# Performance work log

Measured on AMD Instinct MI355X. Metric: run time of the kernel, lower is better.

Reference implementation:

```python
import jax, jax.numpy as jnp
import numpy as np

I_DIM, L_DIM, H_DIM, O_DIM = 1024, 1024, 2048, 512
HALT_H = max(4, H_DIM // 2)
BATCH = 4096


def setup_inputs() -> dict:
    key = jax.random.key(0)
    ks = jax.random.split(key, 14)
    s = 0.02
    gin = I_DIM + O_DIM
    jdim = L_DIM + O_DIM
    return {
        "inputs": jax.random.normal(ks[0], (BATCH, I_DIM), jnp.float32),
        "W_ih": jax.random.normal(ks[1], (3 * L_DIM, gin), jnp.float32) * s,
        "W_hh": jax.random.normal(ks[2], (3 * L_DIM, L_DIM), jnp.float32) * s,
        "b_ih": jax.random.normal(ks[3], (3 * L_DIM,), jnp.float32) * s,
        "b_hh": jax.random.normal(ks[4], (3 * L_DIM,), jnp.float32) * s,
        "aw1": jax.random.normal(ks[5], (H_DIM, jdim), jnp.float32) * s,
        "ab1": jax.random.normal(ks[6], (H_DIM,), jnp.float32) * s,
        "aw2": jax.random.normal(ks[7], (O_DIM, H_DIM), jnp.float32) * s,
        "ab2": jax.random.normal(ks[8], (O_DIM,), jnp.float32) * s,
        "hw1": jax.random.normal(ks[9], (HALT_H, jdim), jnp.float32) * s,
        "hb1": jax.random.normal(ks[10], (HALT_H,), jnp.float32) * s,
        "hw2": jax.random.normal(ks[11], (2, HALT_H), jnp.float32) * s,
        "hb2": jax.random.normal(ks[12], (2,), jnp.float32) * s,
        "inner_cycles": 4,
        "outer_steps": 8,
    }


def reference(inputs, W_ih, W_hh, b_ih, b_hh, aw1, ab1, aw2, ab2,
              hw1, hb1, hw2, hb2, inner_cycles, outer_steps):
    B = inputs.shape[0]
    L = W_hh.shape[1]
    O = aw2.shape[0]

    def gru_step(state, x_gates):
        # PyTorch GRUCell: gates ordered (r, z, n)
        h_gates = state @ W_hh.T + b_hh  # [B, 3L]
        xr, xz, xn = jnp.split(x_gates, 3, axis=-1)
        hr, hz, hn = jnp.split(h_gates, 3, axis=-1)
        r = jax.nn.sigmoid(xr + hr)
        z = jax.nn.sigmoid(xz + hz)
        n = jnp.tanh(xn + r * hn)
        return (1.0 - z) * n + z * state

    def outer(carry, _):
        state, ans = carry
        # gru_input is constant over inner cycles -> hoist input projection
        x = jnp.concatenate([inputs, ans], axis=-1)       # [B, I+O]
        x_gates = x @ W_ih.T + b_ih                        # [B, 3L]

        def inner(s, _):
            return gru_step(s, x_gates), None

        state, _ = jax.lax.scan(inner, state, None, length=inner_cycles)
        joint = jnp.concatenate([state, ans], axis=-1)     # [B, L+O]
        h1 = jax.nn.relu(joint @ aw1.T + ab1)
        logits = h1 @ aw2.T + ab2                          # [B, O]
        ans_new = jnp.tanh(logits)
        h2 = jax.nn.relu(joint @ hw1.T + hb1)
        halt = h2 @ hw2.T + hb2                            # [B, 2]
        return (state, ans_new), (logits, halt)

    state0 = jnp.zeros((B, L), inputs.dtype)
    ans0 = jnp.zeros((B, O), inputs.dtype)
    _, (answer_logits, halt_logits) = jax.lax.scan(
        outer, (state0, ans0), None, length=outer_steps)
    # stacked equivalents of the per-step lists: [outer_steps, B, O], [outer_steps, B, 2]
    return answer_logits, halt_logits
```

## Files before the change

kernel.cpp:

```cpp
#include <hip/hip_runtime.h>
#include <math.h>

#define BATCH 4096
#define LDIM 1024
#define HDIM 2048
#define ODIM 512
#define GDIM 3072
#define JDIM 1536
#define INNER 4
#define OUTER 8

using f16 = _Float16;
using f16x4 = __attribute__((ext_vector_type(4))) _Float16;
using f16x8 = __attribute__((ext_vector_type(8))) _Float16;
using f32x4 = __attribute__((ext_vector_type(4))) float;

typedef __attribute__((address_space(3))) void lds_void;
typedef __attribute__((address_space(1))) void glob_void;

__device__ __forceinline__ void gload16(const void* g, void* l) {
  __builtin_amdgcn_global_load_lds((const glob_void*)g, (lds_void*)l, 16, 0, 0);
}

#define MFMA16(a, b, c) __builtin_amdgcn_mfma_f32_16x16x32_f16(a, b, c, 0, 0, 0)
#define WAIT_VM(N) asm volatile("s_waitcnt vmcnt(" #N ")" ::: "memory")

__device__ __forceinline__ float fast_sigmoid(float x) {
  return __builtin_amdgcn_rcpf(1.0f + __expf(-x));
}
__device__ __forceinline__ float fast_tanh(float x) {
  return 1.0f - 2.0f * __builtin_amdgcn_rcpf(1.0f + __expf(2.0f * x));
}

__global__ __launch_bounds__(256) void convert_w(const float* __restrict__ src,
                                                 f16* __restrict__ dst, int n4) {
  int i = blockIdx.x * 256 + threadIdx.x;
  if (i >= n4) return;
  float4 v = ((const float4*)src)[i];
  f16x4 d = {(f16)v.x, (f16)v.y, (f16)v.z, (f16)v.w};
  *(f16x4*)&dst[(size_t)i * 4] = d;
}

__global__ __launch_bounds__(256) void input_to_cat(
    const float* __restrict__ inp, f16* __restrict__ cH) {
  int idx = blockIdx.x * 256 + threadIdx.x;
  if (idx >= BATCH * 256) return;
  int row = idx >> 8, c4 = idx & 255;
  float4 v = ((const float4*)inp)[idx];
  f16x4 h4 = {(f16)v.x, (f16)v.y, (f16)v.z, (f16)v.w};
  *(f16x4*)&cH[(size_t)row * JDIM + c4 * 4] = h4;
}

template <int EPI>
__global__ __launch_bounds__(256, 2) void gemm_f16(
    const f16* __restrict__ A, const f16* __restrict__ W,
    const float* __restrict__ bias, const float* __restrict__ bias2,
    f16* __restrict__ Ch, float* __restrict__ Cf, float* __restrict__ Cout,
    f16* __restrict__ aXH, f16* __restrict__ aJH, int N, int K) {
  __shared__ f16 sA[3][128 * 32];
  __shared__ f16 sW[3][128 * 32];
  const int tid = threadIdx.x;
  const int w = tid >> 6, lane = tid & 63;
  const int wm = w >> 1, wn = w & 1;
  const int fr = lane & 15, quad = lane >> 4;
  const int m0 = blockIdx.y * 128, n0 = blockIdx.x * 128;
  const int srow = w * 32 + (lane >> 2);
  const int scol = (((lane & 3) ^ ((lane >> 3) & 3)) * 8);
  const f16* pA = A + (size_t)(m0 + srow) * K + scol;
  const f16* pW = W + (size_t)(n0 + srow) * K + scol;
  const size_t rstep = (size_t)16 * K;
  const int lo = w * 1024;

  f32x4 acc[4][4] = {};
  const int NT = K >> 5;

  auto stage = [&](int b, int k) {
    gload16(pA + k, &sA[b][lo]);
    gload16(pA + rstep + k, &sA[b][lo + 512]);
    gload16(pW + k, &sW[b][lo]);
    gload16(pW + rstep + k, &sW[b][lo + 512]);
  };
  stage(0, 0);
  stage(1, 32);
  int bb = 0;
  for (int t = 0; t < NT; ++t) {
    if (t == NT - 1) { WAIT_VM(0); } else { WAIT_VM(4); }
    __builtin_amdgcn_s_barrier();
    if (t + 2 < NT) {
      int bn = bb + 2; if (bn >= 3) bn -= 3;
      stage(bn, (t + 2) * 32);
    }
    f16x8 af[4], bf[4];
#pragma unroll
    for (int i = 0; i < 4; ++i) {
      int rr = wm * 64 + i * 16 + fr;
      af[i] = *(const f16x8*)&sA[bb][rr * 32 + ((quad ^ ((rr >> 1) & 3)) << 3)];
    }
#pragma unroll
    for (int j = 0; j < 4; ++j) {
      int rr = wn * 64 + j * 16 + fr;
      bf[j] = *(const f16x8*)&sW[bb][rr * 32 + ((quad ^ ((rr >> 1) & 3)) << 3)];
    }
    __builtin_amdgcn_s_setprio(1);
#pragma unroll
    for (int i = 0; i < 4; ++i)
#pragma unroll
      for (int j = 0; j < 4; ++j) acc[i][j] = MFMA16(af[i], bf[j], acc[i][j]);
    __builtin_amdgcn_s_setprio(0);
    if (++bb == 3) bb = 0;
  }

  bool is_h1 = true;
  const float* bp = bias;
  int nb0 = n0;
  if (EPI == 1) {
    is_h1 = (n0 < 2048);
    bp = is_h1 ? bias : bias2;
    nb0 = is_h1 ? n0 : n0 - 2048;
  }
#pragma unroll
  for (int j = 0; j < 4; ++j) {
    int n = nb0 + wn * 64 + j * 16 + fr;
    float bv = bp[n];
#pragma unroll
    for (int i = 0; i < 4; ++i) {
      int mb = m0 + wm * 64 + i * 16 + quad * 4;
      if (EPI == 0) {
        f16x4 o = {(f16)(acc[i][j][0] + bv), (f16)(acc[i][j][1] + bv),
                   (f16)(acc[i][j][2] + bv), (f16)(acc[i][j][3] + bv)};
        *(f16x4*)&Ch[((size_t)(mb >> 2) * N + n) * 4] = o;
      } else {
#pragma unroll
        for (int r = 0; r < 4; ++r) {
          int m = mb + r;
          float v = acc[i][j][r] + bv;
          if (EPI == 1) {
            float vr = fmaxf(v, 0.0f);
            if (is_h1)
              Ch[(size_t)m * HDIM + n] = (f16)vr;
            else
              Cf[(size_t)m * LDIM + n] = vr;
          } else {
            Cout[(size_t)m * N + n] = v;
            f16 t = (f16)fast_tanh(v);
            size_t c = (size_t)m * JDIM + 1024 + n;
            aXH[c] = t;
            aJH[c] = t;
          }
        }
      }
    }
  }
}

__global__ __launch_bounds__(256, 2) void gru_fused(
    const f16* __restrict__ inH, const f16* __restrict__ Whh,
    const float* __restrict__ bhh, const f16* __restrict__ xgP,
    f16* __restrict__ outH, f16* __restrict__ catJH) {
  __shared__ f16 sA[3][128 * 32];
  __shared__ f16 sW0[3][64 * 32];
  __shared__ f16 sW1[3][64 * 32];
  __shared__ f16 sW2[3][64 * 32];
  const int tid = threadIdx.x;
  const int w = tid >> 6, lane = tid & 63;
  const int fr = lane & 15, quad = lane >> 4;
  const int n0 = blockIdx.x * 64, m0 = blockIdx.y * 128;
  const int srow = w * 32 + (lane >> 2);
  const int scol = (((lane & 3) ^ ((lane >> 3) & 3)) * 8);
  const f16* pA = inH + (size_t)(m0 + srow) * LDIM + scol;
  const size_t rstepA = (size_t)16 * LDIM;
  const int wrow = w * 16 + (lane >> 2);
  const f16* pW0 = Whh + (size_t)(n0 + wrow) * LDIM + scol;
  const f16* pW1 = pW0 + (size_t)LDIM * LDIM;
  const f16* pW2 = pW1 + (size_t)LDIM * LDIM;
  const int loA = w * 1024, loW = w * 512;

  f32x4 ar[2][4] = {}, az[2][4] = {}, an_[2][4] = {};
  const int NT = LDIM >> 5;

  auto stage = [&](int b, int k) {
    gload16(pA + k, &sA[b][loA]);
    gload16(pA + rstepA + k, &sA[b][loA + 512]);
    gload16(pW0 + k, &sW0[b][loW]);
    gload16(pW1 + k, &sW1[b][loW]);
    gload16(pW2 + k, &sW2[b][loW]);
  };
  stage(0, 0);
  stage(1, 32);
  int bb = 0;
  for (int t = 0; t < NT; ++t) {
    if (t == NT - 1) { WAIT_VM(0); } else { WAIT_VM(5); }
    __builtin_amdgcn_s_barrier();
    if (t + 2 < NT) {
      int bn = bb + 2; if (bn >= 3) bn -= 3;
      stage(bn, (t + 2) * 32);
    }
    f16x8 a_[2], w0[4], w1[4], w2[4];
#pragma unroll
    for (int i = 0; i < 2; ++i) {
      int rr = w * 32 + i * 16 + fr;
      a_[i] = *(const f16x8*)&sA[bb][rr * 32 + ((quad ^ ((rr >> 1) & 3)) << 3)];
    }
#pragma unroll
    for (int j = 0; j < 4; ++j) {
      int rw = j * 16 + fr;
      int wo = rw * 32 + ((quad ^ ((rw >> 1) & 3)) << 3);
      w0[j] = *(const f16x8*)&sW0[bb][wo];
      w1[j] = *(const f16x8*)&sW1[bb][wo];
      w2[j] = *(const f16x8*)&sW2[bb][wo];
    }
    __builtin_amdgcn_s_setprio(1);
#pragma unroll
    for (int i = 0; i < 2; ++i)
#pragma unroll
      for (int j = 0; j < 4; ++j) {
        ar[i][j] = MFMA16(a_[i], w0[j], ar[i][j]);
        az[i][j] = MFMA16(a_[i], w1[j], az[i][j]);
        an_[i][j] = MFMA16(a_[i], w2[j], an_[i][j]);
      }
    __builtin_amdgcn_s_setprio(0);
    if (++bb == 3) bb = 0;
  }

#pragma unroll
  for (int j = 0; j < 4; ++j) {
    int col = n0 + j * 16 + fr;
    float br = bhh[col], bz = bhh[col + LDIM], bn = bhh[col + 2 * LDIM];
#pragma unroll
    for (int i = 0; i < 2; ++i) {
      int mb = m0 + w * 32 + i * 16 + quad * 4;
      size_t xb = ((size_t)(mb >> 2) * GDIM + col) * 4;
      f16x4 x4r = *(const f16x4*)&xgP[xb];
      f16x4 x4z = *(const f16x4*)&xgP[xb + (size_t)LDIM * 4];
      f16x4 x4n = *(const f16x4*)&xgP[xb + (size_t)2 * LDIM * 4];
#pragma unroll
      for (int r = 0; r < 4; ++r) {
        int m = mb + r;
        size_t si = (size_t)m * LDIM + col;
        float sold = (float)inH[si];
        float rg = fast_sigmoid((float)x4r[r] + ar[i][j][r] + br);
        float zg = fast_sigmoid((float)x4z[r] + az[i][j][r] + bz);
        float ng = fast_tanh((float)x4n[r] + rg * (an_[i][j][r] + bn));
        float o = (1.0f - zg) * ng + zg * sold;
        f16 oh = (f16)o;
        outH[si] = oh;
        if (catJH) catJH[(size_t)m * JDIM + col] = oh;
      }
    }
  }
}

__global__ __launch_bounds__(256) void halt_kernel(
    const float* __restrict__ h2, const float* __restrict__ hw2,
    const float* __restrict__ hb2, float* __restrict__ out) {
  int wave = (blockIdx.x * 256 + threadIdx.x) >> 6;
  int lane = threadIdx.x & 63;
  if (wave >= BATCH) return;
  const float* row = h2 + (size_t)wave * LDIM;
  float s0 = 0.0f, s1 = 0.0f;
#pragma unroll
  for (int k = lane; k < LDIM; k += 64) {
    float v = row[k];
    s0 = fmaf(v, hw2[k], s0);
    s1 = fmaf(v, hw2[LDIM + k], s1);
  }
#pragma unroll
  for (int off = 32; off > 0; off >>= 1) {
    s0 += __shfl_xor(s0, off);
    s1 += __shfl_xor(s1, off);
  }
  if (lane == 0) {
    out[(size_t)wave * 2 + 0] = s0 + hb2[0];
    out[(size_t)wave * 2 + 1] = s1 + hb2[1];
  }
}

extern "C" void kernel_launch(void* const* d_in, const int* in_sizes, int n_in,
                              void* d_out, int out_size, void* d_ws, size_t ws_size,
                              hipStream_t stream) {
  const float* inputs = (const float*)d_in[0];
  const float* W_ih = (const float*)d_in[1];
  const float* W_hh = (const float*)d_in[2];
  const float* b_ih = (const float*)d_in[3];
  const float* b_hh = (const float*)d_in[4];
  const float* aw1 = (const float*)d_in[5];
  const float* ab1 = (const float*)d_in[6];
  const float* aw2 = (const float*)d_in[7];
  const float* ab2 = (const float*)d_in[8];
  const float* hw1 = (const float*)d_in[9];
  const float* hb1 = (const float*)d_in[10];
  const float* hw2 = (const float*)d_in[11];
  const float* hb2 = (const float*)d_in[12];

  float* out = (float*)d_out;
  float* logits_out = out;
  float* halt_out = out + (size_t)OUTER * BATCH * ODIM;

  char* p = (char*)d_ws;
  auto take = [&](size_t bytes) { char* q = p; p += (bytes + 255) & ~255ull; return q; };
  f16* stA = (f16*)take((size_t)BATCH * LDIM * 2);
  f16* stB = (f16*)take((size_t)BATCH * LDIM * 2);
  f16* catX = (f16*)take((size_t)BATCH * JDIM * 2);
  f16* catJ = (f16*)take((size_t)BATCH * JDIM * 2);
  f16* xg = (f16*)take((size_t)BATCH * GDIM * 2);
  float* h2F = (float*)take((size_t)BATCH * LDIM * 4);
  f16* WihF = (f16*)take((size_t)GDIM * JDIM * 2);
  f16* WhhF = (f16*)take((size_t)GDIM * LDIM * 2);
  f16* WjF = (f16*)take((size_t)(HDIM + LDIM) * JDIM * 2);
  f16* aw2F = (f16*)take((size_t)ODIM * HDIM * 2);
  f16* h1 = xg;

  (void)hipMemsetAsync(stA, 0, (size_t)BATCH * LDIM * 2, stream);
  (void)hipMemsetAsync(catX, 0, (size_t)BATCH * JDIM * 2, stream);
  (void)hipMemsetAsync(catJ, 0, (size_t)BATCH * JDIM * 2, stream);

  auto conv = [&](const float* s, f16* d, size_t n) {
    int n4 = (int)(n / 4);
    convert_w<<<(n4 + 255) / 256, 256, 0, stream>>>(s, d, n4);
  };
  conv(W_ih, WihF, (size_t)GDIM * JDIM);
  conv(W_hh, WhhF, (size_t)GDIM * LDIM);
  conv(aw1, WjF, (size_t)HDIM * JDIM);
  conv(hw1, WjF + (size_t)HDIM * JDIM, (size_t)LDIM * JDIM);
  conv(aw2, aw2F, (size_t)ODIM * HDIM);
  input_to_cat<<<BATCH, 256, 0, stream>>>(inputs, catX);

  for (int s = 0; s < OUTER; ++s) {
    gemm_f16<0><<<dim3(GDIM / 128, BATCH / 128), 256, 0, stream>>>(
        catX, WihF, b_ih, nullptr, xg, nullptr, nullptr, nullptr, nullptr,
        GDIM, JDIM);
    f16 *cur = stA, *nxt = stB;
    for (int c = 0; c < INNER; ++c) {
      bool last = (c == INNER - 1);
      gru_fused<<<dim3(LDIM / 64, BATCH / 128), 256, 0, stream>>>(
          cur, WhhF, b_hh, xg, nxt, last ? catJ : nullptr);
      f16* t = cur; cur = nxt; nxt = t;
    }
    gemm_f16<1><<<dim3((HDIM + LDIM) / 128, BATCH / 128), 256, 0, stream>>>(
        catJ, WjF, ab1, hb1, h1, h2F, nullptr, nullptr, nullptr,
        HDIM + LDIM, JDIM);
    gemm_f16<2><<<dim3(ODIM / 128, BATCH / 128), 256, 0, stream>>>(
        h1, aw2F, ab2, nullptr, nullptr, nullptr,
        logits_out + (size_t)s * BATCH * ODIM, catX, catJ, ODIM, HDIM);
    halt_kernel<<<BATCH / 4, 256, 0, stream>>>(
        h2F, hw2, hb2, halt_out + (size_t)s * BATCH * 2);
  }
}
```

Baseline: 2.726 ms.

## Enlarge GEMM tiles to 256x128 and remap blocks for XCD-local weight reuse

The main f16 GEMM now uses 256x128 block tiles with 8x4 MFMA accumulators per wave, doubling A-tile reuse per weight load. Block indices are flattened and remapped so each XCD handles a contiguous set of N columns, improving L2 locality of weight tiles; the GRU kernel gets the same XCD-aware remap. The logits GEMM is split into its own kernel keeping the 128x128 tile. Larger tiles raise register and LDS usage, which may reduce occupancy, and 384 blocks may leave the grid less evenly balanced across CUs.

```diff
diff --git a/kernel.cpp b/kernel.cpp
--- a/kernel.cpp
+++ b/kernel.cpp
@@ -55,7 +55,103 @@
 __global__ __launch_bounds__(256, 2) void gemm_f16(
     const f16* __restrict__ A, const f16* __restrict__ W,
     const float* __restrict__ bias, const float* __restrict__ bias2,
-    f16* __restrict__ Ch, float* __restrict__ Cf, float* __restrict__ Cout,
+    f16* __restrict__ Ch, float* __restrict__ Cf, int N, int K) {
+  __shared__ f16 sA[3][256 * 32];
+  __shared__ f16 sW[3][128 * 32];
+  const int tid = threadIdx.x;
+  const int w = tid >> 6, lane = tid & 63;
+  const int wm = w >> 1, wn = w & 1;
+  const int fr = lane & 15, quad = lane >> 4;
+  const int flat = blockIdx.x;
+  const int xcd = flat & 7, local = flat >> 3;
+  const int n0 = (xcd * 3 + local % 3) * 128;
+  const int m0 = (local / 3) * 256;
+  const int srowA = w * 64 + (lane >> 2);
+  const int srowW = w * 32 + (lane >> 2);
+  const int scol = (((lane & 3) ^ ((lane >> 3) & 3)) * 8);
+  const f16* pA = A + (size_t)(m0 + srowA) * K + scol;
+  const f16* pW = W + (size_t)(n0 + srowW) * K + scol;
+  const size_t rstep = (size_t)16 * K;
+  const int loA = w * 2048, loW = w * 1024;
+
+  f32x4 acc[8][4] = {};
+  const int NT = K >> 5;
+
+  auto stage = [&](int b, int k) {
+    gload16(pA + k, &sA[b][loA]);
+    gload16(pA + rstep + k, &sA[b][loA + 512]);
+    gload16(pA + 2 * rstep + k, &sA[b][loA + 1024]);
+    gload16(pA + 3 * rstep + k, &sA[b][loA + 1536]);
+    gload16(pW + k, &sW[b][loW]);
+    gload16(pW + rstep + k, &sW[b][loW + 512]);
+  };
+  stage(0, 0);
+  stage(1, 32);
+  int bb = 0;
+  for (int t = 0; t < NT; ++t) {
+    if (t == NT - 1) { WAIT_VM(0); } else { WAIT_VM(6); }
+    __builtin_amdgcn_s_barrier();
+    if (t + 2 < NT) {
+      int bn = bb + 2; if (bn >= 3) bn -= 3;
+      stage(bn, (t + 2) * 32);
+    }
+    f16x8 af[8], bf[4];
+#pragma unroll
+    for (int i = 0; i < 8; ++i) {
+      int rr = wm * 128 + i * 16 + fr;
+      af[i] = *(const f16x8*)&sA[bb][rr * 32 + ((quad ^ ((rr >> 1) & 3)) << 3)];
+    }
+#pragma unroll
+    for (int j = 0; j < 4; ++j) {
+      int rr = wn * 64 + j * 16 + fr;
+      bf[j] = *(const f16x8*)&sW[bb][rr * 32 + ((quad ^ ((rr >> 1) & 3)) << 3)];
+    }
+    __builtin_amdgcn_s_setprio(1);
+#pragma unroll
+    for (int i = 0; i < 8; ++i)
+#pragma unroll
+      for (int j = 0; j < 4; ++j) acc[i][j] = MFMA16(af[i], bf[j], acc[i][j]);
+    __builtin_amdgcn_s_setprio(0);
+    if (++bb == 3) bb = 0;
+  }
+
+  bool is_h1 = true;
+  const float* bp = bias;
+  int nb0 = n0;
+  if (EPI == 1) {
+    is_h1 = (n0 < 2048);
+    bp = is_h1 ? bias : bias2;
+    nb0 = is_h1 ? n0 : n0 - 2048;
+  }
+#pragma unroll
+  for (int j = 0; j < 4; ++j) {
+    int n = nb0 + wn * 64 + j * 16 + fr;
+    float bv = bp[n];
+#pragma unroll
+    for (int i = 0; i < 8; ++i) {
+      int mb = m0 + wm * 128 + i * 16 + quad * 4;
+      if (EPI == 0) {
+        f16x4 o = {(f16)(acc[i][j][0] + bv), (f16)(acc[i][j][1] + bv),
+                   (f16)(acc[i][j][2] + bv), (f16)(acc[i][j][3] + bv)};
+        *(f16x4*)&Ch[((size_t)(mb >> 2) * N + n) * 4] = o;
+      } else {
+#pragma unroll
+        for (int r = 0; r < 4; ++r) {
+          int m = mb + r;
+          float v = fmaxf(acc[i][j][r] + bv, 0.0f);
+          if (is_h1)
+            Ch[(size_t)m * HDIM + n] = (f16)v;
+          else
+            Cf[(size_t)m * LDIM + n] = v;
+        }
+      }
+    }
+  }
+}
+
+__global__ __launch_bounds__(256, 2) void gemm_logits(
+    const f16* __restrict__ A, const f16* __restrict__ W,
+    const float* __restrict__ bias, float* __restrict__ Cout,
     f16* __restrict__ aXH, f16* __restrict__ aJH, int N, int K) {
   __shared__ f16 sA[3][128 * 32];
   __shared__ f16 sW[3][128 * 32];
@@ -110,44 +206,22 @@
     if (++bb == 3) bb = 0;
   }
 
-  bool is_h1 = true;
-  const float* bp = bias;
-  int nb0 = n0;
-  if (EPI == 1) {
-    is_h1 = (n0 < 2048);
-    bp = is_h1 ? bias : bias2;
-    nb0 = is_h1 ? n0 : n0 - 2048;
-  }
 #pragma unroll
   for (int j = 0; j < 4; ++j) {
-    int n = nb0 + wn * 64 + j * 16 + fr;
-    float bv = bp[n];
+    int n = n0 + wn * 64 + j * 16 + fr;
+    float bv = bias[n];
 #pragma unroll
     for (int i = 0; i < 4; ++i) {
       int mb = m0 + wm * 64 + i * 16 + quad * 4;
-      if (EPI == 0) {
-        f16x4 o = {(f16)(acc[i][j][0] + bv), (f16)(acc[i][j][1] + bv),
-                   (f16)(acc[i][j][2] + bv), (f16)(acc[i][j][3] + bv)};
-        *(f16x4*)&Ch[((size_t)(mb >> 2) * N + n) * 4] = o;
-      } else {
-#pragma unroll
-        for (int r = 0; r < 4; ++r) {
-          int m = mb + r;
-          float v = acc[i][j][r] + bv;
-          if (EPI == 1) {
-            float vr = fmaxf(v, 0.0f);
-            if (is_h1)
-              Ch[(size_t)m * HDIM + n] = (f16)vr;
-            else
-              Cf[(size_t)m * LDIM + n] = vr;
-          } else {
-            Cout[(size_t)m * N + n] = v;
-            f16 t = (f16)fast_tanh(v);
-            size_t c = (size_t)m * JDIM + 1024 + n;
-            aXH[c] = t;
-            aJH[c] = t;
-          }
-        }
+#pragma unroll
+      for (int r = 0; r < 4; ++r) {
+        int m = mb + r;
+        float v = acc[i][j][r] + bv;
+        Cout[(size_t)m * N + n] = v;
+        f16 t = (f16)fast_tanh(v);
+        size_t c = (size_t)m * JDIM + 1024 + n;
+        aXH[c] = t;
+        aJH[c] = t;
       }
     }
   }
@@ -164,7 +238,10 @@
   const int tid = threadIdx.x;
   const int w = tid >> 6, lane = tid & 63;
   const int fr = lane & 15, quad = lane >> 4;
-  const int n0 = blockIdx.x * 64, m0 = blockIdx.y * 128;
+  const int flat = blockIdx.x;
+  const int xcd = flat & 7, local = flat >> 3;
+  const int n0 = (xcd * 2 + (local & 1)) * 64;
+  const int m0 = (local >> 1) * 128;
   const int srow = w * 32 + (lane >> 2);
   const int scol = (((lane & 3) ^ ((lane >> 3) & 3)) * 8);
   const f16* pA = inH + (size_t)(m0 + srow) * LDIM + scol;
@@ -326,22 +403,20 @@
   input_to_cat<<<BATCH, 256, 0, stream>>>(inputs, catX);
 
   for (int s = 0; s < OUTER; ++s) {
-    gemm_f16<0><<<dim3(GDIM / 128, BATCH / 128), 256, 0, stream>>>(
-        catX, WihF, b_ih, nullptr, xg, nullptr, nullptr, nullptr, nullptr,
-        GDIM, JDIM);
+    gemm_f16<0><<<384, 256, 0, stream>>>(
+        catX, WihF, b_ih, nullptr, xg, nullptr, GDIM, JDIM);
     f16 *cur = stA, *nxt = stB;
     for (int c = 0; c < INNER; ++c) {
       bool last = (c == INNER - 1);
-      gru_fused<<<dim3(LDIM / 64, BATCH / 128), 256, 0, stream>>>(
+      gru_fused<<<512, 256, 0, stream>>>(
           cur, WhhF, b_hh, xg, nxt, last ? catJ : nullptr);
       f16* t = cur; cur = nxt; nxt = t;
     }
-    gemm_f16<1><<<dim3((HDIM + LDIM) / 128, BATCH / 128), 256, 0, stream>>>(
-        catJ, WjF, ab1, hb1, h1, h2F, nullptr, nullptr, nullptr,
-        HDIM + LDIM, JDIM);
-    gemm_f16<2><<<dim3(ODIM / 128, BATCH / 128), 256, 0, stream>>>(
-        h1, aw2F, ab2, nullptr, nullptr, nullptr,
-        logits_out + (size_t)s * BATCH * ODIM, catX, catJ, ODIM, HDIM);
+    gemm_f16<1><<<384, 256, 0, stream>>>(
+        catJ, WjF, ab1, hb1, h1, h2F, HDIM + LDIM, JDIM);
+    gemm_logits<<<dim3(ODIM / 128, BATCH / 128), 256, 0, stream>>>(
+        h1, aw2F, ab2, logits_out + (size_t)s * BATCH * ODIM, catX, catJ,
+        ODIM, HDIM);
     halt_kernel<<<BATCH / 4, 256, 0, stream>>>(
         h2F, hw2, hb2, halt_out + (size_t)s * BATCH * 2);
   }
```

After: 2.730 ms. About the same (+0.1%).
